# Kernel tuning notes

Measured on AMD Instinct MI355X. Metric: run time of the kernel, lower is better.

The kernel has to match this reference:

```python
import jax, jax.numpy as jnp
import numpy as np

BETA = 0.25
EPS = 1e-12  # matches torch F.normalize default eps


def l2norm(x):
    # x / max(||x||_2, eps) over last dim, like torch.nn.functional.normalize
    n = jnp.linalg.norm(x, axis=-1, keepdims=True)
    return x / jnp.maximum(n, EPS)


def setup_inputs() -> dict:
    key = jax.random.key(0)
    kz, kw = jax.random.split(key)
    B, C, H, W = 16, 128, 32, 32
    K, D = 8192, 128
    z = jax.random.normal(kz, (B, C, H, W), dtype=jnp.float32)
    # kmeans_init=False path: randn then l2norm
    weight = l2norm(jax.random.normal(kw, (K, D), dtype=jnp.float32))
    return {"z": z, "weight": weight}


def reference(z, weight):
    B, C, H, W = z.shape
    # b c h w -> b h w c, then l2norm over channel dim
    zt = l2norm(jnp.transpose(z, (0, 2, 3, 1)))
    z_flat = zt.reshape(-1, C)                        # (N, D)
    x_sq = jnp.sum(z_flat * z_flat, axis=1, keepdims=True)      # (N, 1)
    c_sq = jnp.sum(weight * weight, axis=1)[None, :]            # (1, K)
    xc = jnp.einsum('nd,kd->nk', z_flat, weight)                # (N, K) GEMM
    dists = x_sq + c_sq - 2.0 * xc
    encoding_indices = jnp.argmin(dists, axis=1)                # (N,)
    z_q = weight[encoding_indices].reshape(zt.shape)            # (B,H,W,C)
    # commitment loss: beta * mse(stop_grad(z_q), z)
    loss = BETA * jnp.mean((jax.lax.stop_gradient(z_q) - zt) ** 2)
    # straight-through estimator
    z_q = zt + jax.lax.stop_gradient(z_q - zt)
    z_q = jnp.transpose(z_q, (0, 3, 1, 2))                      # b h w c -> b c h w
    return z_q, loss, encoding_indices
```

## Files before the change

kernel.cpp:

```cpp
#include <hip/hip_runtime.h>
#include <hip/hip_bf16.h>

typedef unsigned int u32;
typedef unsigned long long u64;
typedef unsigned short u16;

#define NPOS 16384
#define DCH  128
#define KCB  8192
#define HW   1024
#define BETA 0.25f
#define ZQ_SZ 2097152
#define MARGIN 0.022f
#define QCAP 4096
#define ZSTR 132
#define ROWS 64

typedef __attribute__((ext_vector_type(8))) short short8;
typedef __attribute__((ext_vector_type(4))) float f32x4;

#define GLOAD16(G, L) __builtin_amdgcn_global_load_lds( \
    (const __attribute__((address_space(1))) u32*)(const void*)(G), \
    (__attribute__((address_space(3))) u32*)(void*)(L), 16, 0, 0)

__device__ inline u16 f2bf(float x) {
    u32 u = __float_as_uint(x);
    return (u16)((u + 0x7FFFu + ((u >> 16) & 1u)) >> 16);
}
__device__ inline u32 mono(float f) {
    u32 b = __float_as_uint(f);
    return (b & 0x80000000u) ? ~b : (b | 0x80000000u);
}

__global__ __launch_bounds__(256) void kwprep(const float* __restrict__ w,
                                              u16* __restrict__ wb,
                                              float* __restrict__ csq) {
    const int t = threadIdx.x;
    const int row = blockIdx.x * 16 + (t >> 4);
    const int l = t & 15;
    const float4* src = (const float4*)(w + (size_t)row * DCH + l * 8);
    float4 a = src[0], b = src[1];
    float s = a.x*a.x + a.y*a.y + a.z*a.z + a.w*a.w
            + b.x*b.x + b.y*b.y + b.z*b.z + b.w*b.w;
    union { u16 h[8]; uint4 v; } u;
    u.h[0]=f2bf(a.x); u.h[1]=f2bf(a.y); u.h[2]=f2bf(a.z); u.h[3]=f2bf(a.w);
    u.h[4]=f2bf(b.x); u.h[5]=f2bf(b.y); u.h[6]=f2bf(b.z); u.h[7]=f2bf(b.w);
    *(uint4*)(wb + (size_t)row * DCH + l * 8) = u.v;
    s += __shfl_xor(s, 1, 64);
    s += __shfl_xor(s, 2, 64);
    s += __shfl_xor(s, 4, 64);
    s += __shfl_xor(s, 8, 64);
    if (l == 0) csq[row] = s;
}

__global__ __launch_bounds__(512, 2) void kmain(const float* __restrict__ z,
                                                const float* __restrict__ wgt,
                                                const u16* __restrict__ wb,
                                                const float* __restrict__ csq,
                                                float* __restrict__ out) {
    __shared__ __align__(16) u16 Wpriv[8][3][16 * 128];
    __shared__ __align__(16) float ztl[ROWS * ZSTR];
    __shared__ u32 queue[QCAP];
    __shared__ u32 rowMinU[ROWS];
    __shared__ u64 finalkey[ROWS];
    __shared__ float psum[ROWS][8];
    __shared__ float invL[ROWS];
    __shared__ int codes[ROWS];
    __shared__ float lsum[8];
    __shared__ int qcnt;

    const int t = threadIdx.x;
    const int lane = t & 63;
    const int w = t >> 6;
    const int lr = lane & 15, lk = lane >> 4;
    const int n0 = blockIdx.x * ROWS;
    const int b = n0 >> 10, hw0 = n0 & 1023;
    const int p = lane;

    float vch[16];
    {
        const float* zp = z + (size_t)b * DCH * HW + hw0 + p;
        #pragma unroll
        for (int j = 0; j < 16; ++j)
            vch[j] = zp[(size_t)(w * 16 + j) * HW];
        float s = 0.f;
        #pragma unroll
        for (int j = 0; j < 16; ++j) s += vch[j] * vch[j];
        psum[p][w] = s;
    }
    if (t < ROWS) { rowMinU[t] = 0x7f800000u; finalkey[t] = ~0ULL; }
    if (t == 0) qcnt = 0;
    __syncthreads();
    if (t < ROWS) {
        float ss = 0.f;
        #pragma unroll
        for (int j = 0; j < 8; ++j) ss += psum[t][j];
        invL[t] = 1.0f / fmaxf(sqrtf(ss), 1e-12f);
    }
    __syncthreads();
    {
        float inv = invL[p];
        #pragma unroll
        for (int j = 0; j < 16; ++j)
            ztl[p * ZSTR + w * 16 + j] = vch[j] * inv;
    }
    __syncthreads();

    short8 af[4][4];
    #pragma unroll
    for (int rt = 0; rt < 4; ++rt)
        #pragma unroll
        for (int ks = 0; ks < 4; ++ks) {
            int row = rt * 16 + lr;
            int kb = ks * 32 + lk * 8;
            const float4* zr = (const float4*)&ztl[row * ZSTR + kb];
            float4 x0 = zr[0], x1 = zr[1];
            union { u16 h[8]; short8 v; } uu;
            uu.h[0]=f2bf(x0.x); uu.h[1]=f2bf(x0.y); uu.h[2]=f2bf(x0.z); uu.h[3]=f2bf(x0.w);
            uu.h[4]=f2bf(x1.x); uu.h[5]=f2bf(x1.y); uu.h[6]=f2bf(x1.z); uu.h[7]=f2bf(x1.w);
            af[rt][ks] = uu.v;
        }

    u16* mybuf = &Wpriv[w][0][0];

#define STAGE(BUFO, KT) do { \
    const u16* src_ = wb + (size_t)(KT) * 16384 + w * 16 * 128; \
    _Pragma("unroll") \
    for (int q_ = 0; q_ < 4; ++q_) { \
        int rloc_ = q_ * 4 + lk; \
        int c_ = lr ^ (rloc_ & 7); \
        GLOAD16(src_ + rloc_ * 128 + c_ * 8, mybuf + (BUFO) + q_ * 512); \
    } \
} while (0)

#define COMPUTE(BUFO, KT, COLLECT) do { \
    short8 bf_[4]; \
    _Pragma("unroll") \
    for (int ks_ = 0; ks_ < 4; ++ks_) { \
        int slot_ = (ks_ * 4 + lk) ^ (lr & 7); \
        bf_[ks_] = *(const short8*)(mybuf + (BUFO) + lr * 128 + slot_ * 8); \
    } \
    __builtin_amdgcn_s_waitcnt(0  ); \
    STAGE_NEXT; \
    f32x4 acc_[4] = {}; \
    _Pragma("unroll") \
    for (int ks_ = 0; ks_ < 4; ++ks_) { \
        acc_[0] = __builtin_amdgcn_mfma_f32_16x16x32_bf16(af[0][ks_], bf_[ks_], acc_[0], 0, 0, 0); \
        acc_[1] = __builtin_amdgcn_mfma_f32_16x16x32_bf16(af[1][ks_], bf_[ks_], acc_[1], 0, 0, 0); \
        acc_[2] = __builtin_amdgcn_mfma_f32_16x16x32_bf16(af[2][ks_], bf_[ks_], acc_[2], 0, 0, 0); \
        acc_[3] = __builtin_amdgcn_mfma_f32_16x16x32_bf16(af[3][ks_], bf_[ks_], acc_[3], 0, 0, 0); \
    } \
    float hm_ = 1.0f; \
    float dv_[16]; \
    _Pragma("unroll") \
    for (int rt_ = 0; rt_ < 4; ++rt_) \
        _Pragma("unroll") \
        for (int e_ = 0; e_ < 4; ++e_) { \
            int i_ = rt_ * 4 + e_; \
            float d_ = fmaf(acc_[rt_][e_], -2.f, 2.125f); \
            dv_[i_] = d_; \
            bmin[i_] = fminf(bmin[i_], d_); \
            hm_ = fminf(hm_, d_ - thr[i_]); \
        } \
    if (COLLECT && hm_ <= 0.0f) { \
        u32 cd_ = (u32)((KT) * 128 + w * 16 + lr); \
        _Pragma("unroll") \
        for (int rt_ = 0; rt_ < 4; ++rt_) \
            _Pragma("unroll") \
            for (int e_ = 0; e_ < 4; ++e_) { \
                if (dv_[rt_ * 4 + e_] <= thr[rt_ * 4 + e_]) { \
                    u32 rl_ = (u32)(rt_ * 16 + lk * 4 + e_); \
                    int qi_ = atomicAdd(&qcnt, 1); \
                    if (qi_ < QCAP) queue[qi_] = (rl_ << 13) | cd_; \
                } \
            } \
    } \
} while (0)

#define REFRESH() do { \
    _Pragma("unroll") \
    for (int i_ = 0; i_ < 16; ++i_) { \
        float v_ = bmin[i_]; \
        v_ = fminf(v_, __shfl_xor(v_, 1, 64)); \
        v_ = fminf(v_, __shfl_xor(v_, 2, 64)); \
        v_ = fminf(v_, __shfl_xor(v_, 4, 64)); \
        v_ = fminf(v_, __shfl_xor(v_, 8, 64)); \
        if (lr == 0) \
            atomicMin(&rowMinU[(i_ >> 2) * 16 + lk * 4 + (i_ & 3)], __float_as_uint(v_)); \
    } \
    _Pragma("unroll") \
    for (int i_ = 0; i_ < 16; ++i_) \
        thr[i_] = fminf(__uint_as_float(rowMinU[(i_ >> 2) * 16 + lk * 4 + (i_ & 3)]), bmin[i_]) + MARGIN; \
} while (0)

    float bmin[16], thr[16];
    #pragma unroll
    for (int i = 0; i < 16; ++i) { bmin[i] = 3.4e38f; thr[i] = -1.f; }

    STAGE(0, 0);
    STAGE(2048, 1);
    STAGE(4096, 2);
    asm volatile("s_waitcnt vmcnt(8)" ::: "memory");
    __builtin_amdgcn_sched_barrier(0);
#define STAGE_NEXT do {} while (0)
    {
        COMPUTE(0, 0, false);
    }
    asm volatile("s_waitcnt vmcnt(4)" ::: "memory");
    __builtin_amdgcn_sched_barrier(0);
    {
        COMPUTE(2048, 1, false);
    }
#undef STAGE_NEXT
    REFRESH();

    int bufo = 0;
    #pragma unroll 1
    for (int kt = 0; kt < 64; ++kt) {
        asm volatile("s_waitcnt vmcnt(8)" ::: "memory");
        __builtin_amdgcn_sched_barrier(0);
#define STAGE_NEXT STAGE(bufo, (kt + 3) & 63)
        COMPUTE(bufo, kt, true);
#undef STAGE_NEXT
        if ((kt & 7) == 7) REFRESH();
        bufo += 2048;
        if (bufo == 6144) bufo = 0;
    }

    __syncthreads();

    {
        int nq = qcnt < QCAP ? qcnt : QCAP;
        int gq = t >> 4, l = t & 15;
        for (int qi = gq; qi < nq; qi += 32) {
            u32 e = queue[qi];
            int rl = e >> 13;
            int code = e & 0x1FFF;
            const float4* zr = (const float4*)&ztl[rl * ZSTR + l * 8];
            const float4* wr2 = (const float4*)(wgt + (size_t)code * DCH + l * 8);
            float4 za = zr[0], zb = zr[1], wa = wr2[0], wbv = wr2[1];
            float s = 0.f;
            s = fmaf(za.x, wa.x, s); s = fmaf(za.y, wa.y, s);
            s = fmaf(za.z, wa.z, s); s = fmaf(za.w, wa.w, s);
            s = fmaf(zb.x, wbv.x, s); s = fmaf(zb.y, wbv.y, s);
            s = fmaf(zb.z, wbv.z, s); s = fmaf(zb.w, wbv.w, s);
            s += __shfl_xor(s, 1, 64);
            s += __shfl_xor(s, 2, 64);
            s += __shfl_xor(s, 4, 64);
            s += __shfl_xor(s, 8, 64);
            if (l == 0) {
                float ed = csq[code] - 2.0f * s;
                u64 key = ((u64)mono(ed) << 32) | (u32)code;
                atomicMin((unsigned long long*)&finalkey[rl], (unsigned long long)key);
            }
        }
    }
    __syncthreads();

    if (t < ROWS) {
        u32 code = (u32)finalkey[t];
        codes[t] = (int)code;
        out[ZQ_SZ + 1 + n0 + t] = (float)code;
    }
    __syncthreads();
    {
        const float4* wrp = (const float4*)(wgt + (size_t)codes[p] * DCH + w * 16);
        float4 wv0 = wrp[0], wv1 = wrp[1], wv2 = wrp[2], wv3 = wrp[3];
        float wvf[16] = { wv0.x, wv0.y, wv0.z, wv0.w, wv1.x, wv1.y, wv1.z, wv1.w,
                          wv2.x, wv2.y, wv2.z, wv2.w, wv3.x, wv3.y, wv3.z, wv3.w };
        float* ob = out + (size_t)b * DCH * HW + hw0;
        float sq = 0.f;
        #pragma unroll
        for (int j = 0; j < 16; ++j) {
            int c = w * 16 + j;
            float zv = ztl[p * ZSTR + c];
            float diff = wvf[j] - zv;
            ob[(size_t)c * HW + p] = zv + diff;
            sq += diff * diff;
        }
        #pragma unroll
        for (int o = 32; o > 0; o >>= 1) sq += __shfl_down(sq, o, 64);
        if (lane == 0) lsum[w] = sq;
    }
    __syncthreads();
    if (t == 0) {
        float s = lsum[0] + lsum[1] + lsum[2] + lsum[3]
                + lsum[4] + lsum[5] + lsum[6] + lsum[7];
        atomicAdd(out + ZQ_SZ, s * (BETA / (float)ZQ_SZ));
    }

#undef STAGE
#undef COMPUTE
#undef REFRESH
}

extern "C" void kernel_launch(void* const* d_in, const int* in_sizes, int n_in,
                              void* d_out, int out_size, void* d_ws, size_t ws_size,
                              hipStream_t stream) {
    const float* z = (const float*)d_in[0];
    const float* w = (const float*)d_in[1];
    float* out = (float*)d_out;
    float* wsf = (float*)d_ws;

    u16* wb = (u16*)wsf;
    float* csq = wsf + 524288;

    kwprep<<<512, 256, 0, stream>>>(w, wb, csq);
    hipMemsetAsync(out + ZQ_SZ, 0, 4, stream);
    kmain<<<256, 512, 0, stream>>>(z, w, wb, csq, out);
}
```

Before: 164.3 us.

## Filter candidates on raw dot products with running per-row max thresholds

Candidate filtering now compares raw MFMA dot products against a per-row running threshold (best score minus half the margin). It replaces the fused distance conversion and min tracking, adds a cheap per-row-tile max pre-check, and raises the threshold immediately after each enqueue, all to cut VALU work and queue traffic per tile. The weight prefetch moves from after the LDS reads to the top of the loop with a two-tile lookahead, and s_setprio is raised around the MFMA block. Thresholds that tighten within the loop rely on the later exact fp32 rescoring staying correct, and the reduced prefetch depth may expose memory latency.

```diff
diff --git a/kernel.cpp b/kernel.cpp
--- a/kernel.cpp
+++ b/kernel.cpp
@@ -11,7 +11,7 @@
 #define HW   1024
 #define BETA 0.25f
 #define ZQ_SZ 2097152
-#define MARGIN 0.022f
+#define HALFM 0.011f
 #define QCAP 4096
 #define ZSTR 132
 #define ROWS 64
@@ -30,6 +30,10 @@
 __device__ inline u32 mono(float f) {
     u32 b = __float_as_uint(f);
     return (b & 0x80000000u) ? ~b : (b | 0x80000000u);
+}
+__device__ inline float demono(u32 m) {
+    return (m & 0x80000000u) ? __uint_as_float(m ^ 0x80000000u)
+                             : __uint_as_float(~m);
 }
 
 __global__ __launch_bounds__(256) void kwprep(const float* __restrict__ w,
@@ -61,7 +65,7 @@
     __shared__ __align__(16) u16 Wpriv[8][3][16 * 128];
     __shared__ __align__(16) float ztl[ROWS * ZSTR];
     __shared__ u32 queue[QCAP];
-    __shared__ u32 rowMinU[ROWS];
+    __shared__ u32 rowThrU[ROWS];
     __shared__ u64 finalkey[ROWS];
     __shared__ float psum[ROWS][8];
     __shared__ float invL[ROWS];
@@ -88,7 +92,7 @@
         for (int j = 0; j < 16; ++j) s += vch[j] * vch[j];
         psum[p][w] = s;
     }
-    if (t < ROWS) { rowMinU[t] = 0x7f800000u; finalkey[t] = ~0ULL; }
+    if (t < ROWS) { rowThrU[t] = mono(-3.0e38f); finalkey[t] = ~0ULL; }
     if (t == 0) qcnt = 0;
     __syncthreads();
     if (t < ROWS) {
@@ -123,8 +127,14 @@
 
     u16* mybuf = &Wpriv[w][0][0];
 
+    float thra[16], gthr[4];
+    #pragma unroll
+    for (int i = 0; i < 16; ++i) thra[i] = -3.0e38f;
+    #pragma unroll
+    for (int i = 0; i < 4; ++i) gthr[i] = -3.0e38f;
+
 #define STAGE(BUFO, KT) do { \
-    const u16* src_ = wb + (size_t)(KT) * 16384 + w * 16 * 128; \
+    const u16* src_ = wb + (size_t)(KT) * 16384 + w * 2048; \
     _Pragma("unroll") \
     for (int q_ = 0; q_ < 4; ++q_) { \
         int rloc_ = q_ * 4 + lk; \
@@ -140,9 +150,8 @@
         int slot_ = (ks_ * 4 + lk) ^ (lr & 7); \
         bf_[ks_] = *(const short8*)(mybuf + (BUFO) + lr * 128 + slot_ * 8); \
     } \
-    __builtin_amdgcn_s_waitcnt(0  ); \
-    STAGE_NEXT; \
     f32x4 acc_[4] = {}; \
+    __builtin_amdgcn_s_setprio(1); \
     _Pragma("unroll") \
     for (int ks_ = 0; ks_ < 4; ++ks_) { \
         acc_[0] = __builtin_amdgcn_mfma_f32_16x16x32_bf16(af[0][ks_], bf_[ks_], acc_[0], 0, 0, 0); \
@@ -150,81 +159,80 @@
         acc_[2] = __builtin_amdgcn_mfma_f32_16x16x32_bf16(af[2][ks_], bf_[ks_], acc_[2], 0, 0, 0); \
         acc_[3] = __builtin_amdgcn_mfma_f32_16x16x32_bf16(af[3][ks_], bf_[ks_], acc_[3], 0, 0, 0); \
     } \
-    float hm_ = 1.0f; \
-    float dv_[16]; \
+    __builtin_amdgcn_s_setprio(0); \
+    if (COLLECT) { \
+        _Pragma("unroll") \
+        for (int rt_ = 0; rt_ < 4; ++rt_) { \
+            float g_ = fmaxf(fmaxf(acc_[rt_][0], acc_[rt_][1]), \
+                             fmaxf(acc_[rt_][2], acc_[rt_][3])); \
+            if (g_ >= gthr[rt_]) { \
+                u32 cd_ = (u32)((KT) * 128 + w * 16 + lr); \
+                _Pragma("unroll") \
+                for (int e_ = 0; e_ < 4; ++e_) { \
+                    int i_ = rt_ * 4 + e_; \
+                    float a_ = acc_[rt_][e_]; \
+                    if (a_ >= thra[i_]) { \
+                        u32 rl_ = (u32)(rt_ * 16 + lk * 4 + e_); \
+                        int qi_ = atomicAdd(&qcnt, 1); \
+                        if (qi_ < QCAP) queue[qi_] = (rl_ << 13) | cd_; \
+                        thra[i_] = fmaxf(thra[i_], a_ - HALFM); \
+                    } \
+                } \
+                gthr[rt_] = fminf(fminf(thra[rt_*4], thra[rt_*4+1]), \
+                                  fminf(thra[rt_*4+2], thra[rt_*4+3])); \
+            } \
+        } \
+    } else { \
+        _Pragma("unroll") \
+        for (int i_ = 0; i_ < 16; ++i_) \
+            thra[i_] = fmaxf(thra[i_], acc_[i_ >> 2][i_ & 3] - HALFM); \
+    } \
+} while (0)
+
+#define REFRESH() do { \
+    _Pragma("unroll") \
+    for (int i_ = 0; i_ < 16; ++i_) { \
+        float v_ = thra[i_]; \
+        v_ = fmaxf(v_, __shfl_xor(v_, 1, 64)); \
+        v_ = fmaxf(v_, __shfl_xor(v_, 2, 64)); \
+        v_ = fmaxf(v_, __shfl_xor(v_, 4, 64)); \
+        v_ = fmaxf(v_, __shfl_xor(v_, 8, 64)); \
+        thra[i_] = v_; \
+        if (lr == 0) \
+            atomicMax(&rowThrU[(i_ >> 2) * 16 + lk * 4 + (i_ & 3)], mono(v_)); \
+    } \
+    _Pragma("unroll") \
+    for (int i_ = 0; i_ < 16; ++i_) { \
+        u32 mu_ = rowThrU[(i_ >> 2) * 16 + lk * 4 + (i_ & 3)]; \
+        thra[i_] = fmaxf(thra[i_], demono(mu_)); \
+    } \
     _Pragma("unroll") \
     for (int rt_ = 0; rt_ < 4; ++rt_) \
-        _Pragma("unroll") \
-        for (int e_ = 0; e_ < 4; ++e_) { \
-            int i_ = rt_ * 4 + e_; \
-            float d_ = fmaf(acc_[rt_][e_], -2.f, 2.125f); \
-            dv_[i_] = d_; \
-            bmin[i_] = fminf(bmin[i_], d_); \
-            hm_ = fminf(hm_, d_ - thr[i_]); \
-        } \
-    if (COLLECT && hm_ <= 0.0f) { \
-        u32 cd_ = (u32)((KT) * 128 + w * 16 + lr); \
-        _Pragma("unroll") \
-        for (int rt_ = 0; rt_ < 4; ++rt_) \
-            _Pragma("unroll") \
-            for (int e_ = 0; e_ < 4; ++e_) { \
-                if (dv_[rt_ * 4 + e_] <= thr[rt_ * 4 + e_]) { \
-                    u32 rl_ = (u32)(rt_ * 16 + lk * 4 + e_); \
-                    int qi_ = atomicAdd(&qcnt, 1); \
-                    if (qi_ < QCAP) queue[qi_] = (rl_ << 13) | cd_; \
-                } \
-            } \
-    } \
+        gthr[rt_] = fminf(fminf(thra[rt_*4], thra[rt_*4+1]), \
+                          fminf(thra[rt_*4+2], thra[rt_*4+3])); \
 } while (0)
-
-#define REFRESH() do { \
-    _Pragma("unroll") \
-    for (int i_ = 0; i_ < 16; ++i_) { \
-        float v_ = bmin[i_]; \
-        v_ = fminf(v_, __shfl_xor(v_, 1, 64)); \
-        v_ = fminf(v_, __shfl_xor(v_, 2, 64)); \
-        v_ = fminf(v_, __shfl_xor(v_, 4, 64)); \
-        v_ = fminf(v_, __shfl_xor(v_, 8, 64)); \
-        if (lr == 0) \
-            atomicMin(&rowMinU[(i_ >> 2) * 16 + lk * 4 + (i_ & 3)], __float_as_uint(v_)); \
-    } \
-    _Pragma("unroll") \
-    for (int i_ = 0; i_ < 16; ++i_) \
-        thr[i_] = fminf(__uint_as_float(rowMinU[(i_ >> 2) * 16 + lk * 4 + (i_ & 3)]), bmin[i_]) + MARGIN; \
-} while (0)
-
-    float bmin[16], thr[16];
-    #pragma unroll
-    for (int i = 0; i < 16; ++i) { bmin[i] = 3.4e38f; thr[i] = -1.f; }
 
     STAGE(0, 0);
     STAGE(2048, 1);
-    STAGE(4096, 2);
-    asm volatile("s_waitcnt vmcnt(8)" ::: "memory");
-    __builtin_amdgcn_sched_barrier(0);
-#define STAGE_NEXT do {} while (0)
-    {
-        COMPUTE(0, 0, false);
-    }
     asm volatile("s_waitcnt vmcnt(4)" ::: "memory");
     __builtin_amdgcn_sched_barrier(0);
-    {
-        COMPUTE(2048, 1, false);
-    }
-#undef STAGE_NEXT
+    COMPUTE(0, 0, false);
+    asm volatile("s_waitcnt vmcnt(0)" ::: "memory");
+    __builtin_amdgcn_sched_barrier(0);
+    COMPUTE(2048, 1, false);
     REFRESH();
 
-    int bufo = 0;
+    int bufo = 0, sbufo = 4096;
     #pragma unroll 1
     for (int kt = 0; kt < 64; ++kt) {
+        STAGE(sbufo, (kt + 2) & 63);
+        sbufo += 2048; if (sbufo == 6144) sbufo = 0;
+        __builtin_amdgcn_sched_barrier(0);
         asm volatile("s_waitcnt vmcnt(8)" ::: "memory");
         __builtin_amdgcn_sched_barrier(0);
-#define STAGE_NEXT STAGE(bufo, (kt + 3) & 63)
         COMPUTE(bufo, kt, true);
-#undef STAGE_NEXT
+        bufo += 2048; if (bufo == 6144) bufo = 0;
         if ((kt & 7) == 7) REFRESH();
-        bufo += 2048;
-        if (bufo == 6144) bufo = 0;
     }
 
     __syncthreads();
```

Result: no change. 167.0 us (+1.6%).
